# Performance work log

Measured on AMD Instinct MI355X. Metric: run time of the kernel, lower is better.

Reference implementation:

```python
import jax, jax.numpy as jnp
import numpy as np
from jax import lax

T_IN, T_OUT, LATENT, STRIDE = 128, 12, 256, 4

def setup_inputs() -> dict:
    key = jax.random.key(0)
    ks = jax.random.split(key, 6)
    B, L, C = 256, 2048, 12
    X = jax.random.normal(ks[0], (B, L, C), dtype=jnp.float32)
    conv_w = jax.random.normal(ks[1], (LATENT, C, STRIDE), dtype=jnp.float32) / np.sqrt(C * STRIDE)
    conv_b = jnp.zeros((LATENT,), dtype=jnp.float32)
    W_ih = jax.random.normal(ks[2], (3 * LATENT, LATENT), dtype=jnp.float32) / np.sqrt(LATENT)
    W_hh = jax.random.normal(ks[3], (3 * LATENT, LATENT), dtype=jnp.float32) / np.sqrt(LATENT)
    b_ih = jnp.zeros((3 * LATENT,), dtype=jnp.float32)
    b_hh = jnp.zeros((3 * LATENT,), dtype=jnp.float32)
    pred_W = jax.random.normal(ks[4], (T_OUT, LATENT, LATENT), dtype=jnp.float32) / np.sqrt(LATENT)
    pred_b = jnp.zeros((T_OUT, LATENT), dtype=jnp.float32)
    return {"X": X, "conv_w": conv_w, "conv_b": conv_b, "W_ih": W_ih, "W_hh": W_hh,
            "b_ih": b_ih, "b_hh": b_hh, "pred_W": pred_W, "pred_b": pred_b}

def _gru(x_seq, h0, W_ih, W_hh, b_ih, b_hh):
    # x_seq: [T, B, H]; torch nn.GRU equations
    def step(h, x):
        gi = x @ W_ih.T + b_ih
        gh = h @ W_hh.T + b_hh
        i_r, i_z, i_n = jnp.split(gi, 3, axis=-1)
        h_r, h_z, h_n = jnp.split(gh, 3, axis=-1)
        r = jax.nn.sigmoid(i_r + h_r)
        z = jax.nn.sigmoid(i_z + h_z)
        n = jnp.tanh(i_n + r * h_n)
        h_new = (1.0 - z) * n + z * h
        return h_new, h_new
    h_last, outs = lax.scan(step, h0, x_seq)
    return outs, h_last

def reference(X, conv_w, conv_b, W_ih, W_hh, b_ih, b_hh, pred_W, pred_b):
    B = X.shape[0]
    x = jnp.swapaxes(X, 1, 2)                                  # [B, C, L]
    enc = lax.conv_general_dilated(x, conv_w, (STRIDE,), 'VALID',
                                   dimension_numbers=('NCH', 'OIH', 'NCH'))
    enc = enc + conv_b[None, :, None]                          # [B, LATENT, steps]
    enc = jnp.transpose(enc, (2, 0, 1))                        # [steps, B, LATENT]
    # deterministic t = timesteps_in (orig: np.random.randint)
    ctx_in = enc[:T_IN]                                        # [T_IN, B, H]
    h0 = jnp.zeros((B, LATENT), dtype=X.dtype)
    context, h_last = _gru(ctx_in, h0, W_ih, W_hh, b_ih, b_hh)
    enc_s = enc[:T_IN + T_OUT]                                 # [S, B, H], S = 140
    S = T_IN + T_OUT
    cc = context[-1]                                           # [B, H]
    pred = jnp.einsum('bl,kml->kbm', cc, pred_W) + pred_b[:, None, :]   # [K, B, H]
    sim = jnp.einsum('sbl,kcl->ksbc', enc_s, pred)             # [K, S, B, C=B]
    flat = sim.reshape(T_OUT, S * B, B)
    soft = jax.nn.log_softmax(flat, axis=1)                    # normalize over all (step, sample) negatives
    soft_r = soft.reshape(T_OUT, S, B, B)
    kk = jnp.arange(T_OUT)
    sel = soft_r[kk, T_IN + kk]                                # [K, B, B]
    diag = sel[:, jnp.arange(B), jnp.arange(B)]                # [K, B]
    loss = -jnp.sum(diag) / (T_OUT * B)
    idx = jnp.argmax(flat, axis=1)                             # [K, C]
    target = B * (T_IN + kk)[:, None] + jnp.arange(B)[None, :]
    correct = jnp.sum(idx == target).astype(X.dtype)
    accuracy = correct / (B * T_OUT)
    hidden = h_last[None]                                      # [1, B, H] like torch GRU hidden
    return (accuracy, loss, hidden)
```

## Files before the change

### kernel.cpp

```cpp
#include <hip/hip_runtime.h>
#include <hip/hip_fp16.h>


typedef __attribute__((ext_vector_type(4))) float f32x4;
typedef __attribute__((ext_vector_type(8))) _Float16 f16x8;
typedef __attribute__((ext_vector_type(4))) _Float16 f16x4;

__device__ inline float sigm(float x) {
    x = fminf(fmaxf(x, -30.f), 30.f);
    return 1.f / (1.f + __expf(-x));
}
__device__ inline float tanh_(float x) {
    x = fminf(fmaxf(x, -15.f), 15.f);
    float e = __expf(2.f * x);
    return (e - 1.f) / (e + 1.f);
}

__global__ void wprep_kernel(const float* __restrict__ Wih, __half* __restrict__ wh,
                             float* __restrict__ out) {
    int i = blockIdx.x * 256 + threadIdx.x;
    wh[i] = __float2half(Wih[i]);
    if (i < 2) out[i] = 0.f;
}

__global__ void conv_kernel(const float* __restrict__ X, const float* __restrict__ cw,
                            const float* __restrict__ cb, __half* __restrict__ ehi,
                            __half* __restrict__ elo) {
    __shared__ float wt[48 * 256];
    __shared__ float xs[140 * 12];
    int tid = threadIdx.x;
    int tc = blockIdx.x;
    int b  = blockIdx.y;
    for (int i = tid; i < 48 * 256; i += 256) {
        int o = i / 48, cs = i % 48;
        wt[cs * 256 + o] = cw[i];
    }
    int xbase = (b * 2048 + tc * 140) * 12;
    for (int i = tid; i < 1680; i += 256) xs[i] = X[xbase + i];
    __syncthreads();
    int o = tid;
    float bias = cb[o];
    for (int tl = 0; tl < 35; ++tl) {
        float acc = bias;
        #pragma unroll
        for (int cs = 0; cs < 48; ++cs) {
            int c = cs >> 2, s = cs & 3;
            acc += xs[(tl * 4 + s) * 12 + c] * wt[cs * 256 + o];
        }
        int t = tc * 35 + tl;
        size_t m = (size_t)(t * 256 + b);
        __half h = __float2half(acc);
        ehi[m * 256 + o] = h;
        elo[m * 256 + o] = __float2half(acc - __half2float(h));
    }
}

__global__ void gi_gemm(const __half* __restrict__ A, const __half* __restrict__ Bw,
                        const float* __restrict__ bih, const float* __restrict__ bhh,
                        __half* __restrict__ out) {
    int tid = threadIdx.x;
    int lane = tid & 63, wid = tid >> 6;
    int wm = wid >> 1, wn = wid & 1;
    int mbase = blockIdx.x * 128 + wm * 64;
    int nbase = blockIdx.y * 128 + wn * 64;
    int lr = lane & 15, kg = lane >> 4;
    f32x4 acc[4][4];
    #pragma unroll
    for (int i = 0; i < 4; ++i)
        #pragma unroll
        for (int j = 0; j < 4; ++j)
            #pragma unroll
            for (int e = 0; e < 4; ++e) acc[i][j][e] = 0.f;
    #pragma unroll
    for (int kc = 0; kc < 8; ++kc) {
        int ko = kc * 32 + kg * 8;
        f16x8 a[4], bb[4];
        #pragma unroll
        for (int mi = 0; mi < 4; ++mi)
            a[mi] = *(const f16x8*)(A + (size_t)(mbase + mi * 16 + lr) * 256 + ko);
        #pragma unroll
        for (int ni = 0; ni < 4; ++ni)
            bb[ni] = *(const f16x8*)(Bw + (size_t)(nbase + ni * 16 + lr) * 256 + ko);
        #pragma unroll
        for (int mi = 0; mi < 4; ++mi)
            #pragma unroll
            for (int ni = 0; ni < 4; ++ni)
                acc[mi][ni] = __builtin_amdgcn_mfma_f32_16x16x32_f16(a[mi], bb[ni], acc[mi][ni], 0, 0, 0);
    }
    #pragma unroll
    for (int mi = 0; mi < 4; ++mi) {
        int mrow = mbase + mi * 16;
        int t    = mrow >> 8;
        int bblk = (mrow >> 4) & 15;
        #pragma unroll
        for (int ni = 0; ni < 4; ++ni) {
            int j0 = nbase + ni * 16;
            int g  = j0 >> 8;
            int w2 = (j0 & 255) >> 5;
            int q  = (j0 >> 4) & 1;
            int nt = g * 2 + q;
            int j  = j0 + lr;
            float bj = bih[j] + (g < 2 ? bhh[j] : 0.f);
            size_t obase = ((((size_t)t * 16 + bblk) * 8 + w2) * 6 + nt) * 256 + lr * 16 + kg * 4;
            f16x4 pv;
            #pragma unroll
            for (int r = 0; r < 4; ++r)
                pv[r] = (_Float16)(acc[mi][ni][r] + bj);
            *(f16x4*)(out + obase) = pv;
        }
    }
}

__global__ void __launch_bounds__(512, 1)
gru_kernel(const float* __restrict__ Whh, const float* __restrict__ bhh,
           const __half* __restrict__ gi2, float* __restrict__ cc,
           float* __restrict__ out) {
    __shared__ __align__(16) char hb[2][8192];
    int tid = threadIdx.x;
    int lane = tid & 63, w = tid >> 6;
    int n = lane & 15, kg = lane >> 4;
    int bblk = blockIdx.x;

    f16x8 Wf[6][8];
    #pragma unroll
    for (int nt = 0; nt < 6; ++nt) {
        int g = nt >> 1, q = nt & 1;
        int j = g * 256 + w * 32 + q * 16 + n;
        #pragma unroll
        for (int kc = 0; kc < 8; ++kc) {
            const float* wp = Whh + (size_t)j * 256 + kc * 32 + kg * 8;
            f16x8 v;
            #pragma unroll
            for (int e = 0; e < 8; ++e) v[e] = (_Float16)wp[e];
            Wf[nt][kc] = v;
        }
    }
    float bhn[2];
    #pragma unroll
    for (int q = 0; q < 2; ++q) bhn[q] = bhh[512 + w * 32 + q * 16 + n];

    float ho[8];
    #pragma unroll
    for (int i = 0; i < 8; ++i) ho[i] = 0.f;
    for (int i = tid; i < 2048; i += 512) ((int*)hb[0])[i] = 0;

    const __half* gp = gi2 + ((size_t)(bblk * 8 + w) * 6) * 256 + n * 16 + kg * 4;
    f16x4 gc[6], gn[6];
    #pragma unroll
    for (int nt = 0; nt < 6; ++nt) gc[nt] = *(const f16x4*)(gp + nt * 256);
    __syncthreads();

    for (int t = 0; t < 128; ++t) {
        int cur = t & 1, nxt = cur ^ 1;
        const __half* gpn = gp + (size_t)(t + 1) * 196608;
        #pragma unroll
        for (int nt = 0; nt < 6; ++nt) gn[nt] = *(const f16x4*)(gpn + nt * 256);

        f32x4 acc[6];
        #pragma unroll
        for (int nt = 0; nt < 6; ++nt)
            #pragma unroll
            for (int e = 0; e < 4; ++e) acc[nt][e] = 0.f;
        #pragma unroll
        for (int kc = 0; kc < 8; ++kc) {
            int roff = (n * 512 + kc * 64 + kg * 16) ^ ((n & 7) << 4);
            f16x8 a = *(const f16x8*)(hb[cur] + roff);
            #pragma unroll
            for (int nt = 0; nt < 6; ++nt)
                acc[nt] = __builtin_amdgcn_mfma_f32_16x16x32_f16(a, Wf[nt][kc], acc[nt], 0, 0, 0);
        }
        #pragma unroll
        for (int q = 0; q < 2; ++q) {
            int l = w * 32 + q * 16 + n;
            #pragma unroll
            for (int r = 0; r < 4; ++r) {
                float ir  = (float)gc[q][r];
                float iz  = (float)gc[2 + q][r];
                float in_ = (float)gc[4 + q][r];
                float rr = sigm(ir + acc[q][r]);
                float zz = sigm(iz + acc[2 + q][r]);
                float nn = tanh_(in_ + rr * (acc[4 + q][r] + bhn[q]));
                float h = (1.f - zz) * nn + zz * ho[q * 4 + r];
                ho[q * 4 + r] = h;
                int bl = kg * 4 + r;
                int byteoff = (bl * 512 + l * 2) ^ ((bl & 7) << 4);
                *(_Float16*)(hb[nxt] + byteoff) = (_Float16)h;
            }
        }
        #pragma unroll
        for (int nt = 0; nt < 6; ++nt) gc[nt] = gn[nt];
        __syncthreads();
    }
    #pragma unroll
    for (int q = 0; q < 2; ++q) {
        int l = w * 32 + q * 16 + n;
        #pragma unroll
        for (int r = 0; r < 4; ++r) {
            int bg = bblk * 16 + kg * 4 + r;
            float h = ho[q * 4 + r];
            cc[(size_t)bg * 256 + l] = h;
            out[2 + (size_t)bg * 256 + l] = h;
        }
    }
}

__global__ void pred_kernel(const float* __restrict__ cc, const float* __restrict__ pW,
                            const float* __restrict__ pb, float* __restrict__ pred,
                            __half* __restrict__ predh) {
    __shared__ float ccs[16][256];
    int tid = threadIdx.x;
    int cb = blockIdx.x;
    int k  = blockIdx.y;
    int c0 = cb * 16;
    for (int i = tid; i < 16 * 256; i += 256) {
        int cl = i >> 8, l = i & 255;
        ccs[cl][l] = cc[(size_t)(c0 + cl) * 256 + l];
    }
    __syncthreads();
    int m = tid;
    const float4* wrow = (const float4*)(pW + ((size_t)k * 256 + m) * 256);
    float acc[16];
    #pragma unroll
    for (int i = 0; i < 16; ++i) acc[i] = 0.f;
    for (int l4 = 0; l4 < 64; ++l4) {
        float4 wv = wrow[l4];
        #pragma unroll
        for (int cl = 0; cl < 16; ++cl) {
            float4 cv = ((const float4*)ccs[cl])[l4];
            acc[cl] += wv.x * cv.x + wv.y * cv.y + wv.z * cv.z + wv.w * cv.w;
        }
    }
    float bias = pb[k * 256 + m];
    #pragma unroll
    for (int cl = 0; cl < 16; ++cl) {
        float v = acc[cl] + bias;
        size_t idx = ((size_t)k * 256 + c0 + cl) * 256 + m;
        pred[idx] = v;
        predh[idx] = __float2half(v);
    }
}

__global__ void sim_gemm(const __half* __restrict__ A, const __half* __restrict__ P,
                         float* __restrict__ pmax, float* __restrict__ psum,
                         int* __restrict__ pidx) {
    int tid = threadIdx.x;
    int lane = tid & 63, wid = tid >> 6;
    int wm = wid >> 1, wn = wid & 1;
    int mt = blockIdx.x, ct = blockIdx.y, k = blockIdx.z;
    int m0 = mt * 128 + wm * 64;
    int c0 = ct * 128 + wn * 64;
    const __half* Bw = P + (size_t)k * 65536;
    int lr = lane & 15, kg = lane >> 4;
    f32x4 acc[4][4];
    #pragma unroll
    for (int i = 0; i < 4; ++i)
        #pragma unroll
        for (int j = 0; j < 4; ++j)
            #pragma unroll
            for (int e = 0; e < 4; ++e) acc[i][j][e] = 0.f;
    #pragma unroll
    for (int kc = 0; kc < 8; ++kc) {
        int ko = kc * 32 + kg * 8;
        f16x8 a[4], bb[4];
        #pragma unroll
        for (int mi = 0; mi < 4; ++mi)
            a[mi] = *(const f16x8*)(A + (size_t)(m0 + mi * 16 + lr) * 256 + ko);
        #pragma unroll
        for (int ci = 0; ci < 4; ++ci)
            bb[ci] = *(const f16x8*)(Bw + (size_t)(c0 + ci * 16 + lr) * 256 + ko);
        #pragma unroll
        for (int mi = 0; mi < 4; ++mi)
            #pragma unroll
            for (int ci = 0; ci < 4; ++ci)
                acc[mi][ci] = __builtin_amdgcn_mfma_f32_16x16x32_f16(a[mi], bb[ci], acc[mi][ci], 0, 0, 0);
    }
    #pragma unroll
    for (int ci = 0; ci < 4; ++ci) {
        float vmax = -3.0e38f; int vidx = 0;
        #pragma unroll
        for (int mi = 0; mi < 4; ++mi)
            #pragma unroll
            for (int r = 0; r < 4; ++r) {
                float v = acc[mi][ci][r];
                if (v > vmax) { vmax = v; vidx = m0 + mi * 16 + kg * 4 + r; }
            }
        float se = 0.f;
        #pragma unroll
        for (int mi = 0; mi < 4; ++mi)
            #pragma unroll
            for (int r = 0; r < 4; ++r)
                se += __expf(acc[mi][ci][r] - vmax);
        {
            float om = __shfl_xor(vmax, 16); float os = __shfl_xor(se, 16); int oi = __shfl_xor(vidx, 16);
            float nm = fmaxf(vmax, om);
            se = se * __expf(vmax - nm) + os * __expf(om - nm);
            if (om > vmax || (om == vmax && oi < vidx)) vidx = oi;
            vmax = nm;
        }
        {
            float om = __shfl_xor(vmax, 32); float os = __shfl_xor(se, 32); int oi = __shfl_xor(vidx, 32);
            float nm = fmaxf(vmax, om);
            se = se * __expf(vmax - nm) + os * __expf(om - nm);
            if (om > vmax || (om == vmax && oi < vidx)) vidx = oi;
            vmax = nm;
        }
        if (kg == 0) {
            int c = c0 + ci * 16 + lr;
            size_t base = ((size_t)(k * 560 + mt * 2 + wm)) * 256 + c;
            pmax[base] = vmax; psum[base] = se; pidx[base] = vidx;
        }
    }
}

__global__ void fin_kernel(const float* __restrict__ pmax, const float* __restrict__ psum,
                           const int* __restrict__ pidx, const __half* __restrict__ ehi,
                           const __half* __restrict__ elo, const float* __restrict__ pred,
                           float* __restrict__ out) {
    int k = blockIdx.x, c = threadIdx.x;
    float M = -3.0e38f, S = 0.f, bval = -3.0e38f;
    int bidx = 0;
    for (int p = 0; p < 560; ++p) {
        size_t base = ((size_t)(k * 560 + p)) * 256 + c;
        float m = pmax[base], s = psum[base];
        int id = pidx[base];
        if (m > M) { S = S * __expf(M - m) + s; M = m; }
        else       { S += s * __expf(m - M); }
        if (m > bval || (m == bval && id < bidx)) { bval = m; bidx = id; }
    }
    float lse = M + __logf(S);
    const __half* eh = ehi + ((size_t)((128 + k) * 256 + c)) * 256;
    const __half* el = elo + ((size_t)((128 + k) * 256 + c)) * 256;
    const float* pr = pred + ((size_t)(k * 256 + c)) * 256;
    float d = 0.f;
    for (int l = 0; l < 256; ++l)
        d += (__half2float(eh[l]) + __half2float(el[l])) * pr[l];
    float lossp = lse - d;
    int corr = (bidx == (256 * (128 + k) + c)) ? 1 : 0;
    __shared__ float sl[256];
    __shared__ int si[256];
    sl[c] = lossp; si[c] = corr;
    __syncthreads();
    for (int sft = 128; sft > 0; sft >>= 1) {
        if (c < sft) { sl[c] += sl[c + sft]; si[c] += si[c + sft]; }
        __syncthreads();
    }
    if (c == 0) {
        atomicAdd(out + 1, sl[0] / 3072.f);
        atomicAdd(out + 0, ((float)si[0]) / 3072.f);
    }
}

extern "C" void kernel_launch(void* const* d_in, const int* in_sizes, int n_in,
                              void* d_out, int out_size, void* d_ws, size_t ws_size,
                              hipStream_t stream) {
    (void)in_sizes; (void)n_in; (void)out_size; (void)ws_size;
    const float* X   = (const float*)d_in[0];
    const float* cw  = (const float*)d_in[1];
    const float* cb  = (const float*)d_in[2];
    const float* Wih = (const float*)d_in[3];
    const float* Whh = (const float*)d_in[4];
    const float* bih = (const float*)d_in[5];
    const float* bhh = (const float*)d_in[6];
    const float* pW  = (const float*)d_in[7];
    const float* pb  = (const float*)d_in[8];
    float* out = (float*)d_out;

    char* ws = (char*)d_ws;
    size_t o = 0;
    auto alloc = [&](size_t bytes) { char* p = ws + o; o += (bytes + 255) & ~(size_t)255; return p; };
    __half* ehi   = (__half*)alloc(18350080);
    __half* elo   = (__half*)alloc(18350080);
    __half* gi2   = (__half*)alloc(50331648 + 393216);
    __half* wih   = (__half*)alloc(393216);
    float*  ccb   = (float*)alloc(262144);
    float*  pred  = (float*)alloc(3145728);
    __half* predh = (__half*)alloc(1572864);
    float*  pmx   = (float*)alloc(6881280);
    float*  psm   = (float*)alloc(6881280);
    int*    pix   = (int*)alloc(6881280);

    wprep_kernel<<<768, 256, 0, stream>>>(Wih, wih, out);
    conv_kernel<<<dim3(4, 256), 256, 0, stream>>>(X, cw, cb, ehi, elo);
    gi_gemm<<<dim3(256, 6), 256, 0, stream>>>(ehi, wih, bih, bhh, gi2);
    gru_kernel<<<16, 512, 0, stream>>>(Whh, bhh, gi2, ccb, out);
    pred_kernel<<<dim3(16, 12), 256, 0, stream>>>(ccb, pW, pb, pred, predh);
    sim_gemm<<<dim3(280, 2, 12), 256, 0, stream>>>(ehi, predh, pmx, psm, pix);
    fin_kernel<<<12, 256, 0, stream>>>(pmx, psm, pix, ehi, elo, pred, out);
}
```

Baseline: 1.470 ms.

## Split GRU recurrent matmul across 12 waves with shared-memory gate exchange

The GRU kernel now runs 768 threads (12 waves). Each wave computes a quarter of one gate's recurrent product, holding 4 weight tiles instead of 6, and writes the partial results to shared memory. The 8 original waves then read the r/z/n results and do the gate update. This spreads the per-step MFMA work and register-held weights over more waves to shorten the serial 128-step chain, at the cost of an extra shared-memory round trip and a second barrier per step.

```diff
diff --git a/kernel.cpp b/kernel.cpp
--- a/kernel.cpp
+++ b/kernel.cpp
@@ -96,12 +96,12 @@
         for (int ni = 0; ni < 4; ++ni) {
             int j0 = nbase + ni * 16;
             int g  = j0 >> 8;
-            int w2 = (j0 & 255) >> 5;
+            int u2 = (j0 & 255) >> 5;
             int q  = (j0 >> 4) & 1;
             int nt = g * 2 + q;
             int j  = j0 + lr;
             float bj = bih[j] + (g < 2 ? bhh[j] : 0.f);
-            size_t obase = ((((size_t)t * 16 + bblk) * 8 + w2) * 6 + nt) * 256 + lr * 16 + kg * 4;
+            size_t obase = ((((size_t)t * 16 + bblk) * 8 + u2) * 6 + nt) * 256 + lr * 16 + kg * 4;
             f16x4 pv;
             #pragma unroll
             for (int r = 0; r < 4; ++r)
@@ -111,95 +111,114 @@
     }
 }
 
-__global__ void __launch_bounds__(512, 1)
+__global__ void __launch_bounds__(768, 1)
 gru_kernel(const float* __restrict__ Whh, const float* __restrict__ bhh,
            const __half* __restrict__ gi2, float* __restrict__ cc,
            float* __restrict__ out) {
     __shared__ __align__(16) char hb[2][8192];
+    __shared__ __align__(16) float pa[3 * 256 * 16];
     int tid = threadIdx.x;
     int lane = tid & 63, w = tid >> 6;
     int n = lane & 15, kg = lane >> 4;
+    int gq = w >> 2, lq = w & 3;
+    int u = w & 7;
+    bool is_upd = (w < 8);
     int bblk = blockIdx.x;
 
-    f16x8 Wf[6][8];
-    #pragma unroll
-    for (int nt = 0; nt < 6; ++nt) {
-        int g = nt >> 1, q = nt & 1;
-        int j = g * 256 + w * 32 + q * 16 + n;
+    f16x8 Wf[4][8];
+    #pragma unroll
+    for (int q = 0; q < 4; ++q) {
+        int j = gq * 256 + lq * 64 + q * 16 + n;
         #pragma unroll
         for (int kc = 0; kc < 8; ++kc) {
             const float* wp = Whh + (size_t)j * 256 + kc * 32 + kg * 8;
             f16x8 v;
             #pragma unroll
             for (int e = 0; e < 8; ++e) v[e] = (_Float16)wp[e];
-            Wf[nt][kc] = v;
+            Wf[q][kc] = v;
         }
     }
     float bhn[2];
     #pragma unroll
-    for (int q = 0; q < 2; ++q) bhn[q] = bhh[512 + w * 32 + q * 16 + n];
+    for (int q2 = 0; q2 < 2; ++q2) bhn[q2] = bhh[512 + u * 32 + q2 * 16 + n];
 
     float ho[8];
     #pragma unroll
     for (int i = 0; i < 8; ++i) ho[i] = 0.f;
-    for (int i = tid; i < 2048; i += 512) ((int*)hb[0])[i] = 0;
-
-    const __half* gp = gi2 + ((size_t)(bblk * 8 + w) * 6) * 256 + n * 16 + kg * 4;
+    for (int i = tid; i < 2048; i += 768) ((int*)hb[0])[i] = 0;
+
+    const __half* gp = gi2 + ((size_t)(bblk * 8 + u) * 6) * 256 + n * 16 + kg * 4;
     f16x4 gc[6], gn[6];
-    #pragma unroll
-    for (int nt = 0; nt < 6; ++nt) gc[nt] = *(const f16x4*)(gp + nt * 256);
+    if (is_upd) {
+        #pragma unroll
+        for (int nt = 0; nt < 6; ++nt) gc[nt] = *(const f16x4*)(gp + nt * 256);
+    }
     __syncthreads();
 
     for (int t = 0; t < 128; ++t) {
         int cur = t & 1, nxt = cur ^ 1;
-        const __half* gpn = gp + (size_t)(t + 1) * 196608;
-        #pragma unroll
-        for (int nt = 0; nt < 6; ++nt) gn[nt] = *(const f16x4*)(gpn + nt * 256);
-
-        f32x4 acc[6];
-        #pragma unroll
-        for (int nt = 0; nt < 6; ++nt)
-            #pragma unroll
-            for (int e = 0; e < 4; ++e) acc[nt][e] = 0.f;
+        if (is_upd) {
+            const __half* gpn = gp + (size_t)(t + 1) * 196608;
+            #pragma unroll
+            for (int nt = 0; nt < 6; ++nt) gn[nt] = *(const f16x4*)(gpn + nt * 256);
+        }
+        f32x4 acc[4];
+        #pragma unroll
+        for (int q = 0; q < 4; ++q)
+            #pragma unroll
+            for (int e = 0; e < 4; ++e) acc[q][e] = 0.f;
         #pragma unroll
         for (int kc = 0; kc < 8; ++kc) {
             int roff = (n * 512 + kc * 64 + kg * 16) ^ ((n & 7) << 4);
             f16x8 a = *(const f16x8*)(hb[cur] + roff);
             #pragma unroll
-            for (int nt = 0; nt < 6; ++nt)
-                acc[nt] = __builtin_amdgcn_mfma_f32_16x16x32_f16(a, Wf[nt][kc], acc[nt], 0, 0, 0);
-        }
-        #pragma unroll
-        for (int q = 0; q < 2; ++q) {
-            int l = w * 32 + q * 16 + n;
+            for (int q = 0; q < 4; ++q)
+                acc[q] = __builtin_amdgcn_mfma_f32_16x16x32_f16(a, Wf[q][kc], acc[q], 0, 0, 0);
+        }
+        #pragma unroll
+        for (int q = 0; q < 4; ++q) {
+            int l = lq * 64 + q * 16 + n;
+            *(f32x4*)&pa[gq * 4096 + l * 16 + kg * 4] = acc[q];
+        }
+        __syncthreads();
+        if (is_upd) {
+            #pragma unroll
+            for (int q2 = 0; q2 < 2; ++q2) {
+                int l = u * 32 + q2 * 16 + n;
+                f32x4 pr = *(const f32x4*)&pa[l * 16 + kg * 4];
+                f32x4 pz = *(const f32x4*)&pa[4096 + l * 16 + kg * 4];
+                f32x4 pn = *(const f32x4*)&pa[8192 + l * 16 + kg * 4];
+                #pragma unroll
+                for (int r = 0; r < 4; ++r) {
+                    float ir  = (float)gc[q2][r];
+                    float iz  = (float)gc[2 + q2][r];
+                    float in_ = (float)gc[4 + q2][r];
+                    float rr = sigm(ir + pr[r]);
+                    float zz = sigm(iz + pz[r]);
+                    float nn = tanh_(in_ + rr * (pn[r] + bhn[q2]));
+                    float h = (1.f - zz) * nn + zz * ho[q2 * 4 + r];
+                    ho[q2 * 4 + r] = h;
+                    int bl = kg * 4 + r;
+                    int byteoff = (bl * 512 + l * 2) ^ ((bl & 7) << 4);
+                    *(_Float16*)(hb[nxt] + byteoff) = (_Float16)h;
+                }
+            }
+            #pragma unroll
+            for (int nt = 0; nt < 6; ++nt) gc[nt] = gn[nt];
+        }
+        __syncthreads();
+    }
+    if (is_upd) {
+        #pragma unroll
+        for (int q2 = 0; q2 < 2; ++q2) {
+            int l = u * 32 + q2 * 16 + n;
             #pragma unroll
             for (int r = 0; r < 4; ++r) {
-                float ir  = (float)gc[q][r];
-                float iz  = (float)gc[2 + q][r];
-                float in_ = (float)gc[4 + q][r];
-                float rr = sigm(ir + acc[q][r]);
-                float zz = sigm(iz + acc[2 + q][r]);
-                float nn = tanh_(in_ + rr * (acc[4 + q][r] + bhn[q]));
-                float h = (1.f - zz) * nn + zz * ho[q * 4 + r];
-                ho[q * 4 + r] = h;
-                int bl = kg * 4 + r;
-                int byteoff = (bl * 512 + l * 2) ^ ((bl & 7) << 4);
-                *(_Float16*)(hb[nxt] + byteoff) = (_Float16)h;
+                int bg = bblk * 16 + kg * 4 + r;
+                float h = ho[q2 * 4 + r];
+                cc[(size_t)bg * 256 + l] = h;
+                out[2 + (size_t)bg * 256 + l] = h;
             }
-        }
-        #pragma unroll
-        for (int nt = 0; nt < 6; ++nt) gc[nt] = gn[nt];
-        __syncthreads();
-    }
-    #pragma unroll
-    for (int q = 0; q < 2; ++q) {
-        int l = w * 32 + q * 16 + n;
-        #pragma unroll
-        for (int r = 0; r < 4; ++r) {
-            int bg = bblk * 16 + kg * 4 + r;
-            float h = ho[q * 4 + r];
-            cc[(size_t)bg * 256 + l] = h;
-            out[2 + (size_t)bg * 256 + l] = h;
         }
     }
 }
@@ -382,7 +401,7 @@
     wprep_kernel<<<768, 256, 0, stream>>>(Wih, wih, out);
     conv_kernel<<<dim3(4, 256), 256, 0, stream>>>(X, cw, cb, ehi, elo);
     gi_gemm<<<dim3(256, 6), 256, 0, stream>>>(ehi, wih, bih, bhh, gi2);
-    gru_kernel<<<16, 512, 0, stream>>>(Whh, bhh, gi2, ccb, out);
+    gru_kernel<<<16, 768, 0, stream>>>(Whh, bhh, gi2, ccb, out);
     pred_kernel<<<dim3(16, 12), 256, 0, stream>>>(ccb, pW, pb, pred, predh);
     sim_gemm<<<dim3(280, 2, 12), 256, 0, stream>>>(ehi, predh, pmx, psm, pix);
     fin_kernel<<<12, 256, 0, stream>>>(pmx, psm, pix, ehi, elo, pred, out);
```

After: 1.787 ms. 21.6% more time.

## Stage GRU input gates into a triple-buffered LDS ring via async global_load_lds

Applied to the files above, without the earlier changes.

The GRU recurrence kernel no longer prefetches each step's precomputed input-gate values into registers with global loads. It now issues asynchronous global-to-LDS loads two timesteps ahead into a three-slot LDS ring and reads the current step's gates from LDS. The aim is to take global-memory latency off the serial per-step critical path and free registers held by the prefetch buffer. In exchange it uses about 72KB more shared memory and relies on the per-step barrier to order the async LDS writes before they are read. The launch-bounds and waves-per-EU attributes also change, and one unrelated variable is renamed.

```diff
diff --git a/kernel.cpp b/kernel.cpp
--- a/kernel.cpp
+++ b/kernel.cpp
@@ -96,12 +96,12 @@
         for (int ni = 0; ni < 4; ++ni) {
             int j0 = nbase + ni * 16;
             int g  = j0 >> 8;
-            int w2 = (j0 & 255) >> 5;
+            int u2 = (j0 & 255) >> 5;
             int q  = (j0 >> 4) & 1;
             int nt = g * 2 + q;
             int j  = j0 + lr;
             float bj = bih[j] + (g < 2 ? bhh[j] : 0.f);
-            size_t obase = ((((size_t)t * 16 + bblk) * 8 + w2) * 6 + nt) * 256 + lr * 16 + kg * 4;
+            size_t obase = ((((size_t)t * 16 + bblk) * 8 + u2) * 6 + nt) * 256 + lr * 16 + kg * 4;
             f16x4 pv;
             #pragma unroll
             for (int r = 0; r < 4; ++r)
@@ -111,11 +111,12 @@
     }
 }
 
-__global__ void __launch_bounds__(512, 1)
+__global__ __attribute__((amdgpu_waves_per_eu(2, 2))) void __launch_bounds__(512, 2)
 gru_kernel(const float* __restrict__ Whh, const float* __restrict__ bhh,
            const __half* __restrict__ gi2, float* __restrict__ cc,
            float* __restrict__ out) {
     __shared__ __align__(16) char hb[2][8192];
+    __shared__ __align__(16) char gib[3][24576];
     int tid = threadIdx.x;
     int lane = tid & 63, w = tid >> 6;
     int n = lane & 15, kg = lane >> 4;
@@ -144,18 +145,35 @@
     for (int i = 0; i < 8; ++i) ho[i] = 0.f;
     for (int i = tid; i < 2048; i += 512) ((int*)hb[0])[i] = 0;
 
-    const __half* gp = gi2 + ((size_t)(bblk * 8 + w) * 6) * 256 + n * 16 + kg * 4;
-    f16x4 gc[6], gn[6];
-    #pragma unroll
-    for (int nt = 0; nt < 6; ++nt) gc[nt] = *(const f16x4*)(gp + nt * 256);
+    const char* gsrc = (const char*)gi2 + (size_t)bblk * 24576 + w * 3072 + lane * 16;
+    char* gdst = &gib[0][0] + w * 3072;
+    auto stage = [&](int buf, const char* srcp) {
+        #pragma unroll
+        for (int c = 0; c < 3; ++c)
+            __builtin_amdgcn_global_load_lds(
+                (const __attribute__((address_space(1))) void*)(srcp + c * 1024),
+                (__attribute__((address_space(3))) void*)(gdst + buf * 24576 + c * 1024),
+                16, 0, 0);
+    };
+    stage(0, gsrc);
+    stage(1, gsrc + 393216);
+    const char* pref = gsrc + 2 * 393216;
     __syncthreads();
 
+    int cur3 = 0;
     for (int t = 0; t < 128; ++t) {
         int cur = t & 1, nxt = cur ^ 1;
-        const __half* gpn = gp + (size_t)(t + 1) * 196608;
-        #pragma unroll
-        for (int nt = 0; nt < 6; ++nt) gn[nt] = *(const f16x4*)(gpn + nt * 256);
-
+        if (t < 126) {
+            int b2 = cur3 + 2; if (b2 >= 3) b2 -= 3;
+            stage(b2, pref);
+            pref += 393216;
+        }
+        f16x4 gc[6];
+        {
+            const char* gb = &gib[0][0] + cur3 * 24576 + w * 3072 + n * 32 + kg * 8;
+            #pragma unroll
+            for (int nt = 0; nt < 6; ++nt) gc[nt] = *(const f16x4*)(gb + nt * 512);
+        }
         f32x4 acc[6];
         #pragma unroll
         for (int nt = 0; nt < 6; ++nt)
@@ -187,8 +205,7 @@
                 *(_Float16*)(hb[nxt] + byteoff) = (_Float16)h;
             }
         }
-        #pragma unroll
-        for (int nt = 0; nt < 6; ++nt) gc[nt] = gn[nt];
+        cur3 += 1; if (cur3 >= 3) cur3 -= 3;
         __syncthreads();
     }
     #pragma unroll
```

New measurement: 1.474 ms. No clear change (+0.2%).
